# Kernel tuning notes

Hardware: AMD Instinct MI355X
Metric: run time of the kernel (lower is better)

The kernel has to match this reference:

```python
import jax, jax.numpy as jnp
import numpy as np

# Constants derived from init_kwargs (sample_rate=16000, frame_ms=20, hop_ms=None)
SR = 16000
FRAME = 320            # frame_length = int(sr*frame_ms/1000); also NCCF frame_size (frame_time = hop/sr)
HOP = 320
FREQ_LOW, FREQ_HIGH = 85, 3400          # torchaudio detect_pitch_frequency defaults
LAGS = int(np.ceil(SR / FREQ_LOW))      # 189 lags checked
LAG_MIN = int(np.ceil(SR / FREQ_HIGH))  # 5
WIN_MED = 30                            # win_length for median smoothing
EPS = 1e-9


def _nccf(audio):
    """Batched torchaudio _compute_nccf. audio: (B,T) -> (B,K,LAGS)."""
    B, T = audio.shape
    K = -(-T // FRAME)                       # num_of_frames = ceil(T/frame_size)
    p = LAGS + K * FRAME - T                 # right pad
    w = jnp.pad(audio, ((0, 0), (0, p)))
    # seg[b,k,j] = w[b, k*FRAME + j], j in [0, FRAME+LAGS)
    j = jnp.arange(K)[:, None] * FRAME + jnp.arange(FRAME + LAGS)[None, :]
    seg = w[:, j]                            # (B,K,FRAME+LAGS)
    s1 = seg[:, :, :FRAME]                   # (B,K,FRAME)   lag-independent frames
    li = jnp.arange(1, LAGS + 1)[:, None] + jnp.arange(FRAME)[None, :]   # (LAGS,FRAME)
    s2 = seg[:, :, li]                       # (B,K,LAGS,FRAME) shifted frames
    cross = jnp.einsum('bki,bkli->bkl', s1, s2)
    n1 = jnp.sqrt(jnp.einsum('bki,bki->bk', s1, s1))
    n2 = jnp.sqrt(jnp.einsum('bkli,bkli->bkl', s2, s2))
    # torchaudio: sum(s1*s2) / (eps+||s1||)^2 / (eps+||s2||)^2
    return cross / (EPS + n1[..., None]) ** 2 / (EPS + n2) ** 2


def _find_max_per_frame(nccf):
    """torchaudio _find_max_per_frame: prefer smaller near-max lag."""
    tail = nccf[..., LAG_MIN:]
    best_v, best_i = jnp.max(tail, -1), jnp.argmax(tail, -1)
    half_size = nccf.shape[-1] // 2
    half = nccf[..., LAG_MIN:half_size]
    half_v, half_i = jnp.max(half, -1), jnp.argmax(half, -1)
    mask = half_v > 0.99 * best_v
    idx = jnp.where(mask, half_i, best_i)
    return (idx + LAG_MIN + 1).astype(jnp.int32)   # +lag_min, +1 calibration offset


def _median_smoothing(idx):
    """torchaudio _median_smoothing: left replicate-pad, sliding lower-median."""
    pad = (WIN_MED - 1) // 2
    x = jnp.concatenate([jnp.repeat(idx[:, :1], pad, axis=1), idx], axis=1)  # (B,K+pad)
    nwin = x.shape[1] - WIN_MED + 1
    wi = jnp.arange(nwin)[:, None] + jnp.arange(WIN_MED)[None, :]
    win = x[:, wi]                                   # (B,nwin,WIN_MED)
    # torch.median returns the lower median for even window size
    return jnp.sort(win, -1)[..., (WIN_MED - 1) // 2]


def _forward(audio):
    nccf = _nccf(audio)
    idx = _median_smoothing(_find_max_per_frame(nccf))
    f0 = SR / (EPS + idx.astype(jnp.float32))        # (B, K-15)
    voiced = (f0 > 0).astype(jnp.float32)
    T = audio.shape[1]
    Ke = (T - FRAME) // HOP + 1
    fi = jnp.arange(Ke)[:, None] * HOP + jnp.arange(FRAME)[None, :]
    energy = jnp.mean(audio[:, fi] ** 2, axis=-1)    # (B, Ke)
    # train-mode whitening: masked mean/std (ddof=1) over voiced f0
    valid = (f0 > 0).astype(jnp.float32)
    n = jnp.sum(valid)
    mean = jnp.where(n > 0, jnp.sum(f0 * valid) / jnp.maximum(n, 1.0), 0.0)
    var = jnp.sum(((f0 - mean) ** 2) * valid) / jnp.maximum(n - 1.0, 1.0)
    std = jnp.where(n > 1, jnp.sqrt(var), 1.0)
    std = jnp.where(std == 0, 1.0, std)
    whiten = (f0 - mean) / std
    return f0, whiten, voiced, energy


def setup_inputs() -> dict:
    key = jax.random.key(0)
    audio = jax.random.normal(key, (8, 80000), dtype=jnp.float32)
    return {"audio": audio}


def reference(audio):
    # returns (f0_hz, f0_whiten, voiced_prob, energy)
    return _forward(audio)
```

## Files before the change

### kernel.cpp

```cpp
#include <hip/hip_runtime.h>
#include <math.h>

#define SRATE 16000
#define FRAME 320
#define LAGS 189
#define LAG_MIN 5
#define WIN_MED 30
#define BATCH 8
#define TLEN 80000
#define KFRAMES 250
#define NOUT 235
#define NTOT (BATCH * NOUT)
#define SEG (FRAME + LAGS)

__global__ __launch_bounds__(256) void nccf_best_kernel(
    const float* __restrict__ audio, int* __restrict__ best,
    float* __restrict__ out) {
  const int k = blockIdx.x;
  const int b = blockIdx.y;
  const float* row = audio + (size_t)b * TLEN;
  const int base = k * FRAME;

  __shared__ float sh[512];
  __shared__ float Sarr[512];
  __shared__ float pcr[4][192];
  __shared__ float wsum[4];
  __shared__ float shv[192];

  const int tid = threadIdx.x;
  const int w = tid >> 6;
  const int lane = tid & 63;

  if (tid < 128) {
    int j = 4 * tid;
    float4 v;
    if (j + 3 < SEG && base + j + 3 < TLEN) {
      v = *(const float4*)(row + base + j);
    } else {
      v.x = (j + 0 < SEG && base + j + 0 < TLEN) ? row[base + j + 0] : 0.0f;
      v.y = (j + 1 < SEG && base + j + 1 < TLEN) ? row[base + j + 1] : 0.0f;
      v.z = (j + 2 < SEG && base + j + 2 < TLEN) ? row[base + j + 2] : 0.0f;
      v.w = (j + 3 < SEG && base + j + 3 < TLEN) ? row[base + j + 3] : 0.0f;
    }
    *(float4*)&sh[j] = v;
  }
  __syncthreads();

  {
    const int t2 = 2 * tid;
    float x0 = sh[t2], x1 = sh[t2 + 1];
    float sq1 = x1 * x1;
    float incl = x0 * x0 + sq1;
    #pragma unroll
    for (int d = 1; d < 64; d <<= 1) {
      float u = __shfl_up(incl, d, 64);
      if (lane >= d) incl += u;
    }
    if (lane == 63) wsum[w] = incl;
    __syncthreads();
    float off = 0.0f;
    if (w > 0) off += wsum[0];
    if (w > 1) off += wsum[1];
    if (w > 2) off += wsum[2];
    float s_hi = off + incl;
    Sarr[t2 + 1] = s_hi;
    Sarr[t2] = s_hi - sq1;
  }

  if (lane < 48) {
    const int i0b = w * 80;
    float wv[8];
    *(float4*)&wv[0] = *(const float4*)&sh[4 * lane + i0b];
    float cr[4] = {0.f, 0.f, 0.f, 0.f};
    for (int ii = 0; ii < 80; ii += 4) {
      float4 a = *(const float4*)&sh[i0b + ii];
      *(float4*)&wv[4] = *(const float4*)&sh[4 * lane + i0b + ii + 4];
      #pragma unroll
      for (int d = 0; d < 4; ++d) {
        cr[d] += a.x * wv[d + 1] + a.y * wv[d + 2] +
                 a.z * wv[d + 3] + a.w * wv[d + 4];
      }
      wv[0] = wv[4]; wv[1] = wv[5]; wv[2] = wv[6]; wv[3] = wv[7];
    }
    *(float4*)&pcr[w][4 * lane] = *(float4*)cr;
  }
  __syncthreads();

  if (tid < LAGS) {
    float crs = pcr[0][tid] + pcr[1][tid] + pcr[2][tid] + pcr[3][tid];
    float e2s = Sarr[tid + 320] - Sarr[tid];
    if (e2s < 0.0f) e2s = 0.0f;
    float e1s = Sarr[319];
    float d1 = 1e-9f + sqrtf(e1s);
    float d2 = 1e-9f + sqrtf(e2s);
    shv[tid] = crs / (d1 * d1) / (d2 * d2);
    if (tid == 0) out[3 * NTOT + b * KFRAMES + k] = e1s * (1.0f / FRAME);
  }
  __syncthreads();

  if (w == 0) {
    float bv = -INFINITY; int bi = 0;
    float hv = -INFINITY; int hi2 = 0;
    #pragma unroll
    for (int rr = 0; rr < 3; ++rr) {
      int ll = LAG_MIN + lane + 64 * rr;
      if (ll < LAGS) {
        float v = shv[ll];
        if (v > bv || (v == bv && ll < bi)) { bv = v; bi = ll; }
        if (ll < (LAGS / 2) && (v > hv || (v == hv && ll < hi2))) { hv = v; hi2 = ll; }
      }
    }
    #pragma unroll
    for (int off = 32; off >= 1; off >>= 1) {
      float ov = __shfl_xor(bv, off, 64);
      int   oi = __shfl_xor(bi, off, 64);
      if (ov > bv || (ov == bv && oi < bi)) { bv = ov; bi = oi; }
      float ohv = __shfl_xor(hv, off, 64);
      int   ohi = __shfl_xor(hi2, off, 64);
      if (ohv > hv || (ohv == hv && ohi < hi2)) { hv = ohv; hi2 = ohi; }
    }
    if (lane == 0) {
      int chosen = (hv > 0.99f * bv) ? hi2 : bi;
      best[b * KFRAMES + k] = chosen + 1;
    }
  }
}

__global__ __launch_bounds__(256) void median_f0_kernel(
    const int* __restrict__ best, float* __restrict__ out) {
  const int w = blockIdx.x * 4 + (threadIdx.x >> 6);
  const int lane = threadIdx.x & 63;
  const int b = w / NOUT;
  const int t = w - b * NOUT;

  int v = 0x7fffffff;
  if (lane < WIN_MED) {
    int j = t + lane - 14;
    if (j < 0) j = 0;
    v = best[b * KFRAMES + j];
  }
  int c_lt = 0, c_le = 0;
  #pragma unroll
  for (int j = 0; j < WIN_MED; ++j) {
    int bv = __shfl(v, j, 64);
    c_lt += (bv < v) ? 1 : 0;
    c_le += (bv <= v) ? 1 : 0;
  }
  bool cond = (lane < WIN_MED) && (c_lt <= 14) && (c_le > 14);
  unsigned long long m = __ballot(cond);
  int sel = __ffsll((long long)m) - 1;
  int med = __shfl(v, sel, 64);
  if (lane == 0) {
    float f0 = 16000.0f / (1e-9f + (float)med);
    out[b * NOUT + t] = f0;
    out[2 * NTOT + b * NOUT + t] = 1.0f;
  }
}

__global__ __launch_bounds__(256) void whiten_kernel(float* __restrict__ out) {
  __shared__ double red[256];
  __shared__ double red2[256];
  const int t = threadIdx.x;
  double s = 0.0, s2 = 0.0;
  for (int i = t; i < NTOT; i += 256) {
    double f = (double)out[i];
    s += f; s2 += f * f;
  }
  red[t] = s; red2[t] = s2;
  __syncthreads();
  for (int st = 128; st > 0; st >>= 1) {
    if (t < st) { red[t] += red[t + st]; red2[t] += red2[t + st]; }
    __syncthreads();
  }
  __shared__ float fmean_s, finvsd_s;
  if (t == 0) {
    const double n = (double)NTOT;
    double mean = red[0] / n;
    double var = (red2[0] - n * mean * mean) / (n - 1.0);
    if (var < 0.0) var = 0.0;
    double sd = sqrt(var);
    fmean_s = (float)mean;
    finvsd_s = (sd == 0.0) ? 1.0f : (float)(1.0 / sd);
  }
  __syncthreads();
  float fmean = fmean_s, finvsd = finvsd_s;
  for (int i = t; i < NTOT; i += 256) {
    out[NTOT + i] = (out[i] - fmean) * finvsd;
  }
}

extern "C" void kernel_launch(void* const* d_in, const int* in_sizes, int n_in,
                              void* d_out, int out_size, void* d_ws, size_t ws_size,
                              hipStream_t stream) {
  const float* audio = (const float*)d_in[0];
  float* out = (float*)d_out;
  int* best = (int*)d_ws;

  dim3 g1(KFRAMES, BATCH);
  nccf_best_kernel<<<g1, 256, 0, stream>>>(audio, best, out);
  median_f0_kernel<<<(NTOT + 3) / 4, 256, 0, stream>>>(best, out);
  whiten_kernel<<<1, 256, 0, stream>>>(out);
}
```

Before: 72.66 us.

## Unroll cross-correlation loop, fuse NCCF normalize with argmax, widen whiten reduction

The cross-correlation inner loop is fully unrolled with rotating float4 registers in place of the shifted register-array copy. The per-lag normalization is merged into a three-wave argmax using shuffles plus a small shared combine, which drops one barrier and the shv buffer. The whiten kernel moves to 1024 threads with a wave-shuffle reduction and keeps its loaded values in registers so out is not read a second time. The combined argmax keeps smallest-index tie-breaking by using sentinel indices.

New measurement: 72.79 us. No clear change (+0.2%).

```diff
diff --git a/kernel.cpp b/kernel.cpp
--- a/kernel.cpp
+++ b/kernel.cpp
@@ -25,7 +25,8 @@
   __shared__ float Sarr[512];
   __shared__ float pcr[4][192];
   __shared__ float wsum[4];
-  __shared__ float shv[192];
+  __shared__ float pbv[4]; __shared__ int pbi[4];
+  __shared__ float phv[4]; __shared__ int phi[4];
 
   const int tid = threadIdx.x;
   const int w = tid >> 6;
@@ -69,46 +70,51 @@
 
   if (lane < 48) {
     const int i0b = w * 80;
-    float wv[8];
-    *(float4*)&wv[0] = *(const float4*)&sh[4 * lane + i0b];
+    const float* wp = &sh[4 * lane + i0b];
     float cr[4] = {0.f, 0.f, 0.f, 0.f};
-    for (int ii = 0; ii < 80; ii += 4) {
-      float4 a = *(const float4*)&sh[i0b + ii];
-      *(float4*)&wv[4] = *(const float4*)&sh[4 * lane + i0b + ii + 4];
-      #pragma unroll
-      for (int d = 0; d < 4; ++d) {
-        cr[d] += a.x * wv[d + 1] + a.y * wv[d + 2] +
-                 a.z * wv[d + 3] + a.w * wv[d + 4];
-      }
-      wv[0] = wv[4]; wv[1] = wv[5]; wv[2] = wv[6]; wv[3] = wv[7];
-    }
+    float4 w0 = *(const float4*)wp;
+    float4 w1, w2, w3;
+    #define CR_STEP(A, LO, HI)                                         \
+      cr[0] += A.x * LO.y + A.y * LO.z + A.z * LO.w + A.w * HI.x;      \
+      cr[1] += A.x * LO.z + A.y * LO.w + A.z * HI.x + A.w * HI.y;      \
+      cr[2] += A.x * LO.w + A.y * HI.x + A.z * HI.y + A.w * HI.z;      \
+      cr[3] += A.x * HI.x + A.y * HI.y + A.z * HI.z + A.w * HI.w;
+    #pragma unroll
+    for (int ii = 0; ii < 80; ii += 16) {
+      float4 a;
+      a = *(const float4*)&sh[i0b + ii];
+      w1 = *(const float4*)(wp + ii + 4);
+      CR_STEP(a, w0, w1);
+      a = *(const float4*)&sh[i0b + ii + 4];
+      w2 = *(const float4*)(wp + ii + 8);
+      CR_STEP(a, w1, w2);
+      a = *(const float4*)&sh[i0b + ii + 8];
+      w3 = *(const float4*)(wp + ii + 12);
+      CR_STEP(a, w2, w3);
+      a = *(const float4*)&sh[i0b + ii + 12];
+      w0 = *(const float4*)(wp + ii + 16);
+      CR_STEP(a, w3, w0);
+    }
+    #undef CR_STEP
     *(float4*)&pcr[w][4 * lane] = *(float4*)cr;
   }
   __syncthreads();
 
-  if (tid < LAGS) {
-    float crs = pcr[0][tid] + pcr[1][tid] + pcr[2][tid] + pcr[3][tid];
-    float e2s = Sarr[tid + 320] - Sarr[tid];
-    if (e2s < 0.0f) e2s = 0.0f;
-    float e1s = Sarr[319];
-    float d1 = 1e-9f + sqrtf(e1s);
-    float d2 = 1e-9f + sqrtf(e2s);
-    shv[tid] = crs / (d1 * d1) / (d2 * d2);
-    if (tid == 0) out[3 * NTOT + b * KFRAMES + k] = e1s * (1.0f / FRAME);
-  }
-  __syncthreads();
-
-  if (w == 0) {
-    float bv = -INFINITY; int bi = 0;
-    float hv = -INFINITY; int hi2 = 0;
-    #pragma unroll
-    for (int rr = 0; rr < 3; ++rr) {
-      int ll = LAG_MIN + lane + 64 * rr;
-      if (ll < LAGS) {
-        float v = shv[ll];
-        if (v > bv || (v == bv && ll < bi)) { bv = v; bi = ll; }
-        if (ll < (LAGS / 2) && (v > hv || (v == hv && ll < hi2))) { hv = v; hi2 = ll; }
-      }
+  {
+    float bv = -INFINITY; int bi = 999;
+    float hv = -INFINITY; int hi2 = 999;
+    const int ll = (w << 6) + lane;
+    if (w < 3 && ll < LAGS) {
+      float crs = pcr[0][ll] + pcr[1][ll] + pcr[2][ll] + pcr[3][ll];
+      float e2s = Sarr[ll + 320] - Sarr[ll];
+      if (e2s < 0.0f) e2s = 0.0f;
+      float e1s = Sarr[319];
+      float d1 = 1e-9f + sqrtf(e1s);
+      float d2 = 1e-9f + sqrtf(e2s);
+      float v = crs / (d1 * d1) / (d2 * d2);
+      if (ll >= LAG_MIN) { bv = v; bi = ll; }
+      if (ll >= LAG_MIN && ll < (LAGS / 2)) { hv = v; hi2 = ll; }
+      if (tid == 0) out[3 * NTOT + b * KFRAMES + k] = e1s * (1.0f / FRAME);
     }
     #pragma unroll
     for (int off = 32; off >= 1; off >>= 1) {
@@ -119,8 +125,17 @@
       int   ohi = __shfl_xor(hi2, off, 64);
       if (ohv > hv || (ohv == hv && ohi < hi2)) { hv = ohv; hi2 = ohi; }
     }
-    if (lane == 0) {
-      int chosen = (hv > 0.99f * bv) ? hi2 : bi;
+    if (lane == 0) { pbv[w] = bv; pbi[w] = bi; phv[w] = hv; phi[w] = hi2; }
+    __syncthreads();
+    if (tid == 0) {
+      float Bv = pbv[0]; int Bi = pbi[0];
+      float Hv = phv[0]; int Hi = phi[0];
+      #pragma unroll
+      for (int j2 = 1; j2 < 3; ++j2) {
+        if (pbv[j2] > Bv || (pbv[j2] == Bv && pbi[j2] < Bi)) { Bv = pbv[j2]; Bi = pbi[j2]; }
+        if (phv[j2] > Hv || (phv[j2] == Hv && phi[j2] < Hi)) { Hv = phv[j2]; Hi = phi[j2]; }
+      }
+      int chosen = (Hv > 0.99f * Bv) ? Hi : Bi;
       best[b * KFRAMES + k] = chosen + 1;
     }
   }
@@ -157,26 +172,33 @@
   }
 }
 
-__global__ __launch_bounds__(256) void whiten_kernel(float* __restrict__ out) {
-  __shared__ double red[256];
-  __shared__ double red2[256];
+__global__ __launch_bounds__(1024) void whiten_kernel(float* __restrict__ out) {
+  __shared__ double reds[16], reds2[16];
+  __shared__ float fmean_s, finvsd_s;
   const int t = threadIdx.x;
   double s = 0.0, s2 = 0.0;
-  for (int i = t; i < NTOT; i += 256) {
-    double f = (double)out[i];
-    s += f; s2 += f * f;
-  }
-  red[t] = s; red2[t] = s2;
-  __syncthreads();
-  for (int st = 128; st > 0; st >>= 1) {
-    if (t < st) { red[t] += red[t + st]; red2[t] += red2[t + st]; }
-    __syncthreads();
-  }
-  __shared__ float fmean_s, finvsd_s;
+  float fv[2] = {0.f, 0.f};
+  int nv = 0;
+  for (int i = t; i < NTOT; i += 1024) {
+    float f = out[i];
+    fv[nv++] = f;
+    double d = (double)f;
+    s += d; s2 += d * d;
+  }
+  #pragma unroll
+  for (int off = 32; off >= 1; off >>= 1) {
+    s  += __shfl_down(s,  off, 64);
+    s2 += __shfl_down(s2, off, 64);
+  }
+  if ((t & 63) == 0) { reds[t >> 6] = s; reds2[t >> 6] = s2; }
+  __syncthreads();
   if (t == 0) {
+    double S = 0.0, S2 = 0.0;
+    #pragma unroll
+    for (int i = 0; i < 16; ++i) { S += reds[i]; S2 += reds2[i]; }
     const double n = (double)NTOT;
-    double mean = red[0] / n;
-    double var = (red2[0] - n * mean * mean) / (n - 1.0);
+    double mean = S / n;
+    double var = (S2 - n * mean * mean) / (n - 1.0);
     if (var < 0.0) var = 0.0;
     double sd = sqrt(var);
     fmean_s = (float)mean;
@@ -184,8 +206,9 @@
   }
   __syncthreads();
   float fmean = fmean_s, finvsd = finvsd_s;
-  for (int i = t; i < NTOT; i += 256) {
-    out[NTOT + i] = (out[i] - fmean) * finvsd;
+  nv = 0;
+  for (int i = t; i < NTOT; i += 1024) {
+    out[NTOT + i] = (fv[nv++] - fmean) * finvsd;
   }
 }
 
@@ -199,5 +222,5 @@
   dim3 g1(KFRAMES, BATCH);
   nccf_best_kernel<<<g1, 256, 0, stream>>>(audio, best, out);
   median_f0_kernel<<<(NTOT + 3) / 4, 256, 0, stream>>>(best, out);
-  whiten_kernel<<<1, 256, 0, stream>>>(out);
-}
+  whiten_kernel<<<1, 1024, 0, stream>>>(out);
+}
```
